# Kernel tuning notes

Hardware: AMD Instinct MI355X
Metric: run time of the kernel (lower is better)

## Reference

```python
import jax, jax.numpy as jnp
import numpy as np

C = 64
N_H = 4
N_WIN = 16
WIN_L = 8   # compressor window length (overlapped)
WIN_S = 4   # compressor stride -> T//4 blocks


def _rms(x, eps=1e-6):
    return x * jax.lax.rsqrt(jnp.mean(x * x, axis=-1, keepdims=True) + eps)


def _rope(x, negate=False):
    # x: (..., L, D); rotate-half RoPE over positions 0..L-1
    L, D = x.shape[-2], x.shape[-1]
    half = D // 2
    inv_freq = 1.0 / (10000.0 ** (jnp.arange(half, dtype=x.dtype) / half))
    ang = jnp.arange(L, dtype=x.dtype)[:, None] * inv_freq  # (L, half)
    if negate:
        ang = -ang
    cos, sin = jnp.cos(ang), jnp.sin(ang)
    x1, x2 = x[..., :half], x[..., half:]
    return jnp.concatenate([x1 * cos - x2 * sin, x1 * sin + x2 * cos], axis=-1)


def _compress(H, W):
    # overlapped token compressor: windows of WIN_L, stride WIN_S, zero-pad tail
    B, T, d = H.shape
    Tc = T // WIN_S
    Hp = jnp.pad(H, ((0, 0), (0, WIN_L - WIN_S), (0, 0)))
    idx = WIN_S * jnp.arange(Tc)[:, None] + jnp.arange(WIN_L)[None, :]  # (Tc, WIN_L)
    win = Hp[:, idx]                       # (B, Tc, WIN_L, d)
    return win.reshape(B, Tc, WIN_L * d) @ W  # (B, Tc, out)


def setup_inputs() -> dict:
    key = jax.random.key(0)
    ks = jax.random.split(key, 11)
    B, T, d = 2, 2048, 256

    def w(k, shape, fan):
        return jax.random.normal(k, shape, jnp.float32) / np.float32(np.sqrt(fan))

    H = jax.random.normal(ks[0], (B, T, d), jnp.float32)
    return {
        'H': H,
        'Wc_comp': w(ks[1], (WIN_L * d, C), WIN_L * d),
        'Wc_idx': w(ks[2], (WIN_L * d, 32), WIN_L * d),
        'W_DQ': w(ks[3], (d, 64), d),
        'W_IUQ': w(ks[4], (64, 4 * 32), 64),
        'W_w': w(ks[5], (64, 4), 64),
        'W_Q': w(ks[6], (d, N_H * C), d),
        'W_KV': w(ks[7], (d, C), d),
        'g_q': jnp.ones((N_H, C), jnp.float32),
        'g_k': jnp.ones((C,), jnp.float32),
        'g_v': jnp.ones((C,), jnp.float32),
        'Wg0': w(ks[8], (2 * C, 64), 2 * C),
        'bg0': jnp.zeros((64,), jnp.float32),
        'Wg1': w(ks[9], (2 * C, 64), 2 * C),
        'bg1': jnp.zeros((64,), jnp.float32),
        'Wout': w(ks[10], (128, d), 128),
        'bout': jnp.zeros((d,), jnp.float32),
    }


def reference(H, Wc_comp, Wc_idx, W_DQ, W_IUQ, W_w, W_Q, W_KV,
              g_q, g_k, g_v, Wg0, bg0, Wg1, bg1, Wout, bout):
    B, T, d = H.shape
    Tc = T // 4
    k_top = min(8, Tc)

    # ---- lightning indexer ----
    H_dc = H @ W_DQ                                   # (B,T,64)
    Q_I = (H_dc @ W_IUQ).reshape(B, T, 4, 32)         # (B,T,4,32)
    W_Iw = (H_dc @ W_w)[..., None]                    # (B,T,4,1)
    K_I = _compress(H, Wc_idx)                        # (B,Tc,32)
    dot = jnp.einsum('bthc,bsc->bths', Q_I, K_I)      # (B,T,4,Tc)
    I_ts = (W_Iw * jax.nn.relu(dot)).sum(axis=2)      # (B,T,Tc)

    t = jnp.arange(T)[:, None]
    s = jnp.arange(Tc)[None, :]
    mask_I = jnp.where(4 * s <= t, 0.0, -jnp.inf)     # (T,Tc) causal over blocks
    _, topk_idx = jax.lax.top_k(I_ts + mask_I, k_top)  # (B,T,k)
    bI = jnp.arange(B)[:, None, None]
    tI = jnp.arange(T)[None, :, None]
    M_comp = jnp.full((B, T, Tc), -jnp.inf).at[bI, tI, topk_idx].set(0.0)

    # ---- compressed + sliding KV ----
    KV = jnp.concatenate([_compress(H, Wc_comp), H @ W_KV], axis=1)  # (B,Tc+T,C)

    Q = (H @ W_Q).reshape(B, T, N_H, C).transpose(0, 2, 1, 3)        # (B,nh,T,C)
    Q = _rms(Q) * g_q[None, :, None, :]
    K = _rms(KV) * g_k
    V = _rms(KV) * g_v
    Q = _rope(Q)
    K = _rope(K)
    V = _rope(V)

    S = jnp.einsum('bhtc,bsc->bhts', Q, K) / np.float32(np.sqrt(C))  # (B,nh,T,Tc+T)

    S_comp = S[..., :Tc] + M_comp[:, None]
    rel = t - jnp.arange(T)[None, :]
    mask_slide = jnp.where((rel >= 0) & (rel < N_WIN), 0.0, -jnp.inf)  # (T,T)
    S_slide = S[..., Tc:] + mask_slide

    P = jax.nn.softmax(jnp.concatenate([S_comp, S_slide], axis=-1), axis=-1)
    O = jnp.einsum('bhts,bsc->bhtc', P, V)            # (B,nh,T,C)
    O = _rope(O, negate=True)

    O0 = O[:, :2].transpose(0, 2, 1, 3).reshape(B, T, 2 * C)
    O1 = O[:, 2:].transpose(0, 2, 1, 3).reshape(B, T, 2 * C)
    p_all = jnp.concatenate([O0 @ Wg0 + bg0, O1 @ Wg1 + bg1], axis=-1)
    return p_all @ Wout + bout
```

## Files before the change

kernel.cpp:

```cpp
#include <hip/hip_runtime.h>
#include <hip/hip_bf16.h>
#include <math.h>

#define T_DIM 2048
#define B_DIM 2
#define D_DIM 256
#define TC 512
#define KV_LEN 2560

typedef __attribute__((ext_vector_type(8))) short bf16x8;
typedef __attribute__((ext_vector_type(4))) float f32x4;
typedef unsigned short ush;

__device__ __forceinline__ float wave_sum64(float v) {
#pragma unroll
    for (int off = 32; off > 0; off >>= 1) v += __shfl_xor(v, off, 64);
    return v;
}

__device__ __forceinline__ float rope_angle(int pos, int j) {
    float inv = powf(10000.0f, -(float)j * (1.0f / 32.0f));
    return (float)pos * inv;
}

__global__ __launch_bounds__(256) void k_prep(
    const float* __restrict__ H, const float* __restrict__ W_Q,
    const float* __restrict__ W_KV, const float* __restrict__ W_DQ,
    const float* __restrict__ W_IUQ, const float* __restrict__ W_w,
    const float* __restrict__ Wc_comp, const float* __restrict__ Wc_idx,
    const float* __restrict__ Wg0, const float* __restrict__ bg0,
    const float* __restrict__ Wg1, const float* __restrict__ bg1,
    const float* __restrict__ Wout, const float* __restrict__ bout,
    ush* __restrict__ Ap, ush* __restrict__ Bp, ush* __restrict__ Bc,
    ush* __restrict__ Bo, float* __restrict__ biascomb)
{
    int gid = blockIdx.x * 256 + threadIdx.x;
    float vals[8];
    ush* dst;
    bool lo_part;

    if (gid < 262144) {
        int tile = gid >> 10;
        int c = (gid >> 6) & 15;
        int l = gid & 63;
        int bt = tile * 16 + (l & 15);
        int kb = (c & 7) * 32 + (l >> 4) * 8;
        const float* src = H + (size_t)bt * 256 + kb;
#pragma unroll
        for (int j = 0; j < 8; ++j) vals[j] = src[j];
        lo_part = (c >= 8);
        dst = Ap + (size_t)gid * 8;
    } else if (gid < 294912) {
        int g = gid - 262144;
        int tile = g >> 10;
        int c = (g >> 6) & 15;
        int l = g & 63;
        int n = tile * 16 + (l & 15);
        int kb = (c & 7) * 32 + (l >> 4) * 8;
#pragma unroll
        for (int j = 0; j < 8; ++j) {
            int k = kb + j;
            float w;
            if (n < 256)      w = W_Q[(size_t)k * 256 + n];
            else if (n < 320) w = W_KV[(size_t)k * 64 + (n - 256)];
            else if (n < 448) {
                w = 0.f;
                for (int i = 0; i < 64; ++i)
                    w = fmaf(W_DQ[(size_t)k * 64 + i], W_IUQ[(size_t)i * 128 + (n - 320)], w);
            } else if (n < 452) {
                w = 0.f;
                for (int i = 0; i < 64; ++i)
                    w = fmaf(W_DQ[(size_t)k * 64 + i], W_w[(size_t)i * 4 + (n - 448)], w);
            } else {
                w = 0.f;
            }
            vals[j] = w;
        }
        lo_part = (c >= 8);
        dst = Bp + (size_t)g * 8;
    } else if (gid < 344064) {
        int g = gid - 294912;
        int tile = g >> 13;
        int c = (g >> 6) & 127;
        int l = g & 63;
        int n = tile * 16 + (l & 15);
        int k2b = (c & 63) * 32 + (l >> 4) * 8;
#pragma unroll
        for (int j = 0; j < 8; ++j) {
            int k = k2b + j;
            vals[j] = (n < 64) ? Wc_comp[(size_t)k * 64 + n]
                               : Wc_idx[(size_t)k * 32 + (n - 64)];
        }
        lo_part = (c >= 64);
        dst = Bc + (size_t)g * 8;
    } else if (gid < 409600) {
        int g = gid - 344064;
        int k = g >> 8;
        int n = g & 255;
        float acc = 0.f;
        if (k < 128) {
            for (int i = 0; i < 64; ++i)
                acc = fmaf(Wg0[k * 64 + i], Wout[(size_t)i * 256 + n], acc);
        } else {
            for (int i = 0; i < 64; ++i)
                acc = fmaf(Wg1[(k - 128) * 64 + i], Wout[(size_t)(64 + i) * 256 + n], acc);
        }
        __hip_bfloat16 hb = __float2bfloat16(acc);
        float hif = __bfloat162float(hb);
        __hip_bfloat16 lb = __float2bfloat16(acc - hif);
        int tile = n >> 4;
        int chi = k >> 5;
        int lane2 = (n & 15) + 16 * ((k >> 3) & 3);
        int j = k & 7;
        Bo[(size_t)(tile * 16 + chi) * 512 + lane2 * 8 + j] = *(ush*)&hb;
        Bo[(size_t)(tile * 16 + chi + 8) * 512 + lane2 * 8 + j] = *(ush*)&lb;
        return;
    } else if (gid < 409856) {
        int n = gid - 409600;
        float acc = bout[n];
        for (int i = 0; i < 64; ++i) {
            acc = fmaf(bg0[i], Wout[(size_t)i * 256 + n], acc);
            acc = fmaf(bg1[i], Wout[(size_t)(64 + i) * 256 + n], acc);
        }
        biascomb[n] = acc;
        return;
    } else {
        return;
    }

    bf16x8 out8;
#pragma unroll
    for (int j = 0; j < 8; ++j) {
        float x = vals[j];
        __hip_bfloat16 hb = __float2bfloat16(x);
        if (!lo_part) {
            out8[j] = *(short*)&hb;
        } else {
            float hif = __bfloat162float(hb);
            __hip_bfloat16 lb = __float2bfloat16(x - hif);
            out8[j] = *(short*)&lb;
        }
    }
    *(bf16x8*)dst = out8;
}

__global__ __launch_bounds__(64) void k_mfma(
    const ush* __restrict__ Ap, const ush* __restrict__ Bp,
    const ush* __restrict__ Bc,
    const float* __restrict__ g_q, const float* __restrict__ g_k,
    const float* __restrict__ g_v,
    float* __restrict__ Pre, float* __restrict__ Prec_part,
    float* __restrict__ Qr, float* __restrict__ Kbuf, float* __restrict__ Vbuf)
{
    int lane = threadIdx.x;
    int mrow = lane & 15;
    int q = lane >> 4;

    if (blockIdx.x < 512) {
        int p = blockIdx.x;
        int m0 = (p >> 2) * 32;
        int nq = p & 3;
        int n0 = nq * 128;
        int at0 = (m0 >> 4) * 16;
        int bt0n = (n0 >> 4) * 16;

        f32x4 acc[2][8];
#pragma unroll
        for (int mt = 0; mt < 2; ++mt)
#pragma unroll
            for (int nt = 0; nt < 8; ++nt) acc[mt][nt] = (f32x4){0.f, 0.f, 0.f, 0.f};

        for (int c = 0; c < 8; ++c) {
            bf16x8 ahi[2], alo[2], bhi[8], blo[8];
#pragma unroll
            for (int mt = 0; mt < 2; ++mt) {
                ahi[mt] = *(const bf16x8*)(Ap + (size_t)((at0 + mt * 16) + c) * 512 + lane * 8);
                alo[mt] = *(const bf16x8*)(Ap + (size_t)((at0 + mt * 16) + 8 + c) * 512 + lane * 8);
            }
#pragma unroll
            for (int nt = 0; nt < 8; ++nt) {
                bhi[nt] = *(const bf16x8*)(Bp + (size_t)((bt0n + nt * 16) + c) * 512 + lane * 8);
                blo[nt] = *(const bf16x8*)(Bp + (size_t)((bt0n + nt * 16) + 8 + c) * 512 + lane * 8);
            }
#pragma unroll
            for (int mt = 0; mt < 2; ++mt)
#pragma unroll
                for (int nt = 0; nt < 8; ++nt) {
                    acc[mt][nt] = __builtin_amdgcn_mfma_f32_16x16x32_bf16(ahi[mt], bhi[nt], acc[mt][nt], 0, 0, 0);
                    acc[mt][nt] = __builtin_amdgcn_mfma_f32_16x16x32_bf16(ahi[mt], blo[nt], acc[mt][nt], 0, 0, 0);
                    acc[mt][nt] = __builtin_amdgcn_mfma_f32_16x16x32_bf16(alo[mt], bhi[nt], acc[mt][nt], 0, 0, 0);
                }
        }

        if (nq < 2) {
            int h0 = nq * 2, h1 = nq * 2 + 1;
#pragma unroll
            for (int mt = 0; mt < 2; ++mt)
#pragma unroll
                for (int reg = 0; reg < 4; ++reg) {
                    int bt = m0 + 16 * mt + 4 * q + reg;
                    int t = bt & 2047;
                    float ss0 = 0.f, ss1 = 0.f;
#pragma unroll
                    for (int k = 0; k < 4; ++k) {
                        float v0 = acc[mt][k][reg];
                        float v1 = acc[mt][4 + k][reg];
                        ss0 = fmaf(v0, v0, ss0);
                        ss1 = fmaf(v1, v1, ss1);
                    }
#pragma unroll
                    for (int off = 1; off <= 8; off <<= 1) {
                        ss0 += __shfl_xor(ss0, off, 64);
                        ss1 += __shfl_xor(ss1, off, 64);
                    }
                    float sc0 = rsqrtf(ss0 * (1.0f / 64.0f) + 1e-6f);
                    float sc1 = rsqrtf(ss1 * (1.0f / 64.0f) + 1e-6f);
#pragma unroll
                    for (int k = 0; k < 2; ++k) {
                        int jj = 16 * k + mrow;
                        float sa, ca;
                        sincosf(rope_angle(t, jj), &sa, &ca);
                        {
                            float x1 = acc[mt][k][reg] * sc0 * g_q[h0 * 64 + jj];
                            float x2 = acc[mt][k + 2][reg] * sc0 * g_q[h0 * 64 + 32 + jj];
                            Qr[(size_t)bt * 256 + h0 * 64 + jj] = fmaf(x1, ca, -x2 * sa);
                            Qr[(size_t)bt * 256 + h0 * 64 + 32 + jj] = fmaf(x1, sa, x2 * ca);
                        }
                        {
                            float x1 = acc[mt][4 + k][reg] * sc1 * g_q[h1 * 64 + jj];
                            float x2 = acc[mt][4 + k + 2][reg] * sc1 * g_q[h1 * 64 + 32 + jj];
                            Qr[(size_t)bt * 256 + h1 * 64 + jj] = fmaf(x1, ca, -x2 * sa);
                            Qr[(size_t)bt * 256 + h1 * 64 + 32 + jj] = fmaf(x1, sa, x2 * ca);
                        }
                    }
                }
        } else if (nq == 2) {
#pragma unroll
            for (int mt = 0; mt < 2; ++mt)
#pragma unroll
                for (int reg = 0; reg < 4; ++reg) {
                    int bt = m0 + 16 * mt + 4 * q + reg;
                    int b = bt >> 11;
                    int t = bt & 2047;
                    float ss = 0.f;
#pragma unroll
                    for (int k = 0; k < 4; ++k) {
                        float v = acc[mt][k][reg];
                        ss = fmaf(v, v, ss);
                    }
#pragma unroll
                    for (int off = 1; off <= 8; off <<= 1) ss += __shfl_xor(ss, off, 64);
                    float sc = rsqrtf(ss * (1.0f / 64.0f) + 1e-6f);
                    int pos = TC + t;
                    size_t base = ((size_t)b * KV_LEN + pos) * 64;
#pragma unroll
                    for (int k = 0; k < 2; ++k) {
                        int jj = 16 * k + mrow;
                        float sa, ca;
                        sincosf(rope_angle(pos, jj), &sa, &ca);
                        float k1 = acc[mt][k][reg] * sc * g_k[jj];
                        float k2 = acc[mt][k + 2][reg] * sc * g_k[32 + jj];
                        float v1 = acc[mt][k][reg] * sc * g_v[jj];
                        float v2 = acc[mt][k + 2][reg] * sc * g_v[32 + jj];
                        Kbuf[base + jj] = fmaf(k1, ca, -k2 * sa);
                        Kbuf[base + 32 + jj] = fmaf(k1, sa, k2 * ca);
                        Vbuf[base + jj] = fmaf(v1, ca, -v2 * sa);
                        Vbuf[base + 32 + jj] = fmaf(v1, sa, v2 * ca);
                    }
#pragma unroll
                    for (int nt = 4; nt < 8; ++nt)
                        Pre[(size_t)bt * 512 + n0 + 16 * nt + mrow] = acc[mt][nt][reg];
                }
        } else {
#pragma unroll
            for (int mt = 0; mt < 2; ++mt)
#pragma unroll
                for (int nt = 0; nt < 8; ++nt)
#pragma unroll
                    for (int reg = 0; reg < 4; ++reg)
                        Pre[(size_t)(m0 + 16 * mt + 4 * q + reg) * 512 + n0 + 16 * nt + mrow] =
                            acc[mt][nt][reg];
        }
    } else {
        int cb = blockIdx.x - 512;
        int m0 = (cb >> 2) * 32;
        int q4 = cb & 3;
        int bb = m0 >> 9;

        f32x4 acc[2][6];
#pragma unroll
        for (int mt = 0; mt < 2; ++mt)
#pragma unroll
            for (int nt = 0; nt < 6; ++nt) acc[mt][nt] = (f32x4){0.f, 0.f, 0.f, 0.f};

        for (int cl = 0; cl < 16; ++cl) {
            int cc = q4 * 16 + cl;
            int k2b = cc * 32 + q * 8;
            int row_off = k2b >> 8;
            int kcb = k2b & 255;
            int chA = kcb >> 5;
            int lsub = (kcb >> 3) & 3;

            bf16x8 ahi[2], alo[2], bhi[6], blo[6];
#pragma unroll
            for (int mt = 0; mt < 2; ++mt) {
                int s_loc = (m0 & 511) + 16 * mt + mrow;
                int r_loc = 4 * s_loc + row_off;
                int r_glob = bb * 2048 + r_loc;
                int tileA = r_glob >> 4;
                int laneA = (r_glob & 15) + 16 * lsub;
                bf16x8 h8 = *(const bf16x8*)(Ap + (size_t)(tileA * 16 + chA) * 512 + laneA * 8);
                bf16x8 l8 = *(const bf16x8*)(Ap + (size_t)(tileA * 16 + chA + 8) * 512 + laneA * 8);
                if (r_loc >= T_DIM) {
#pragma unroll
                    for (int j = 0; j < 8; ++j) { h8[j] = 0; l8[j] = 0; }
                }
                ahi[mt] = h8;
                alo[mt] = l8;
            }
#pragma unroll
            for (int nt = 0; nt < 6; ++nt) {
                bhi[nt] = *(const bf16x8*)(Bc + (size_t)(nt * 128 + cc) * 512 + lane * 8);
                blo[nt] = *(const bf16x8*)(Bc + (size_t)(nt * 128 + 64 + cc) * 512 + lane * 8);
            }
#pragma unroll
            for (int mt = 0; mt < 2; ++mt)
#pragma unroll
                for (int nt = 0; nt < 6; ++nt) {
                    acc[mt][nt] = __builtin_amdgcn_mfma_f32_16x16x32_bf16(ahi[mt], bhi[nt], acc[mt][nt], 0, 0, 0);
                    acc[mt][nt] = __builtin_amdgcn_mfma_f32_16x16x32_bf16(ahi[mt], blo[nt], acc[mt][nt], 0, 0, 0);
                    acc[mt][nt] = __builtin_amdgcn_mfma_f32_16x16x32_bf16(alo[mt], bhi[nt], acc[mt][nt], 0, 0, 0);
                }
        }

        float* dst = Prec_part + (size_t)q4 * (1024 * 96);
#pragma unroll
        for (int mt = 0; mt < 2; ++mt)
#pragma unroll
            for (int nt = 0; nt < 6; ++nt)
#pragma unroll
                for (int reg = 0; reg < 4; ++reg)
                    dst[(size_t)(m0 + 16 * mt + 4 * q + reg) * 96 + 16 * nt + mrow] =
                        acc[mt][nt][reg];
    }
}

__global__ __launch_bounds__(256) void k_epi(
    const float* __restrict__ Prec_part,
    const float* __restrict__ g_k, const float* __restrict__ g_v,
    float* __restrict__ KIbuf, float* __restrict__ Kbuf, float* __restrict__ Vbuf)
{
    int tid = threadIdx.x;
    int wv = tid >> 6;
    int lane = tid & 63;
    int sg = blockIdx.x * 4 + wv;
    int b = sg >> 9;
    int s = sg & 511;

    const float* p0 = Prec_part + (size_t)sg * 96;
    float kvv = p0[lane] + p0[98304 + lane] + p0[2 * 98304 + lane] + p0[3 * 98304 + lane];

    float ss = wave_sum64(kvv * kvv);
    float sc = rsqrtf(ss * (1.0f / 64.0f) + 1e-6f);
    float kk = kvv * sc * g_k[lane];
    float vv = kvv * sc * g_v[lane];
    int j = lane & 31;
    float sa, ca;
    sincosf(rope_angle(s, j), &sa, &ca);
    float pk = __shfl_xor(kk, 32, 64);
    float pv = __shfl_xor(vv, 32, 64);
    float ko = (lane < 32) ? fmaf(kk, ca, -pk * sa) : fmaf(pk, sa, kk * ca);
    float vo = (lane < 32) ? fmaf(vv, ca, -pv * sa) : fmaf(pv, sa, vv * ca);
    size_t off = ((size_t)b * KV_LEN + s) * 64 + lane;
    Kbuf[off] = ko;
    Vbuf[off] = vo;

    if (lane < 32) {
        float a = p0[64 + lane] + p0[98304 + 64 + lane] +
                  p0[2 * 98304 + 64 + lane] + p0[3 * 98304 + 64 + lane];
        KIbuf[((size_t)b * TC + s) * 32 + lane] = a;
    }
}

__global__ __launch_bounds__(256) void k_score_topk(
    const float* __restrict__ Pre, const float* __restrict__ KIbuf,
    int* __restrict__ topk)
{
    int tid = threadIdx.x;
    int wv = tid >> 6;
    int lane = tid & 63;
    int bt0 = blockIdx.x * 4;
    int bt = bt0 + wv;
    int b = bt >> 11;
    int t = bt & 2047;

    __shared__ float sQ[4][128];
    __shared__ float sw[4][4];
    __shared__ float sKI[64 * 33];

    const float* pr = Pre + (size_t)bt * 512;
    sQ[wv][lane] = pr[320 + lane];
    sQ[wv][64 + lane] = pr[384 + lane];
    if (lane < 4) sw[wv][lane] = pr[448 + lane];

    const float* KIb = KIbuf + (size_t)b * TC * 32;
    int smax = t >> 2;
    int smax_blk = ((bt0 + 3) & 2047) >> 2;

    float vals[8];
#pragma unroll
    for (int r = 0; r < 8; ++r) vals[r] = -INFINITY;

    for (int r = 0; r < 8; ++r) {
        if (r * 64 > smax_blk) break;
        __syncthreads();
        for (int i = tid; i < 512; i += 256) {
            int row = i >> 3;
            int cseg = (i & 7) * 4;
            float4 v = *(const float4*)(KIb + (size_t)(r * 64 + row) * 32 + cseg);
            float* dstp = &sKI[row * 33 + cseg];
            dstp[0] = v.x; dstp[1] = v.y; dstp[2] = v.z; dstp[3] = v.w;
        }
        __syncthreads();

        int s = r * 64 + lane;
        if (s <= smax) {
            float dd0 = 0.f, dd1 = 0.f, dd2 = 0.f, dd3 = 0.f;
#pragma unroll
            for (int c = 0; c < 32; ++c) {
                float kv = sKI[lane * 33 + c];
                dd0 = fmaf(sQ[wv][c], kv, dd0);
                dd1 = fmaf(sQ[wv][32 + c], kv, dd1);
                dd2 = fmaf(sQ[wv][64 + c], kv, dd2);
                dd3 = fmaf(sQ[wv][96 + c], kv, dd3);
            }
            vals[r] = sw[wv][0] * fmaxf(dd0, 0.f) + sw[wv][1] * fmaxf(dd1, 0.f) +
                      sw[wv][2] * fmaxf(dd2, 0.f) + sw[wv][3] * fmaxf(dd3, 0.f);
        }
    }

    unsigned consumed = 0u;
    for (int k2 = 0; k2 < 8; ++k2) {
        float bv = -INFINITY;
        int bi = 0x7fffffff;
#pragma unroll
        for (int r = 0; r < 8; ++r) {
            if (!(consumed & (1u << r))) {
                int s = lane + 64 * r;
                float v = vals[r];
                if (v > bv || (v == bv && s < bi)) { bv = v; bi = s; }
            }
        }
#pragma unroll
        for (int off = 1; off < 64; off <<= 1) {
            float ov = __shfl_xor(bv, off, 64);
            int oi = __shfl_xor(bi, off, 64);
            if (ov > bv || (ov == bv && oi < bi)) { bv = ov; bi = oi; }
        }
        if ((bi & 63) == lane) consumed |= 1u << (bi >> 6);
        if (lane == 0) topk[(size_t)bt * 8 + k2] = bi;
    }
}

__global__ __launch_bounds__(1024) void k_attn(
    const float* __restrict__ Qr, const float* __restrict__ Kbuf,
    const float* __restrict__ Vbuf, const int* __restrict__ topk,
    float* __restrict__ Obuf)
{
    int tid = threadIdx.x;
    int lt = tid >> 8;
    int t256 = tid & 255;
    int h = t256 >> 6;
    int lane = tid & 63;
    int bt0 = blockIdx.x * 4;
    int bt = bt0 + lt;
    int b = bt >> 11;
    int t = bt & 2047;
    int t0 = bt0 & 2047;

    __shared__ float sKV[102 * 65];
    __shared__ float sQ[4][256];
    __shared__ int sPos[4][8];
    __shared__ float sP[4][4][24];

    sQ[lt][t256] = Qr[(size_t)bt * 256 + t256];
    if (t256 < 8) sPos[lt][t256] = topk[(size_t)bt * 8 + t256];
    __syncthreads();

    for (int i = tid; i < 1632; i += 1024) {
        int row = i >> 4;
        int seg = (i & 15) << 2;
        const float* srcbase;
        bool ok = true;
        if (row < 38) {
            int idx = (row < 19) ? row : row - 19;
            int sp = t0 - 15 + idx;
            ok = (sp >= 0);
            srcbase = ((row < 19) ? Kbuf : Vbuf) +
                      ((size_t)b * KV_LEN + TC + sp) * 64;
        } else {
            int r = row - 38;
            int ltt = r >> 4;
            int slot = r & 15;
            int pos = sPos[ltt][slot & 7];
            srcbase = ((slot < 8) ? Kbuf : Vbuf) +
                      ((size_t)b * KV_LEN + pos) * 64;
        }
        if (ok) {
            float4 v = *(const float4*)(srcbase + seg);
            float* d = &sKV[row * 65 + seg];
            d[0] = v.x; d[1] = v.y; d[2] = v.z; d[3] = v.w;
        }
    }
    __syncthreads();

    float scv = -INFINITY;
    if (lane < 24) {
        int krow;
        bool valid;
        if (lane < 8) { krow = 38 + lt * 16 + lane; valid = true; }
        else          { krow = lt + 23 - lane; valid = (t - (lane - 8) >= 0); }
        if (valid) {
            float dd = 0.f;
#pragma unroll
            for (int c = 0; c < 64; ++c)
                dd = fmaf(sQ[lt][h * 64 + c], sKV[krow * 65 + c], dd);
            scv = dd * 0.125f;
        }
    }
    float m = scv;
#pragma unroll
    for (int off = 1; off < 64; off <<= 1) m = fmaxf(m, __shfl_xor(m, off, 64));
    float p = expf(scv - m);
    if (scv == -INFINITY) p = 0.f;
    float l = p;
#pragma unroll
    for (int off = 1; off < 64; off <<= 1) l += __shfl_xor(l, off, 64);
    p /= l;
    if (lane < 24) sP[lt][h][lane] = p;

    float o = 0.f;
#pragma unroll
    for (int j2 = 0; j2 < 8; ++j2) {
        int vrow = 38 + lt * 16 + 8 + j2;
        o = fmaf(sP[lt][h][j2], sKV[vrow * 65 + lane], o);
    }
#pragma unroll
    for (int j2 = 8; j2 < 24; ++j2) {
        if (t - (j2 - 8) >= 0) {
            int vrow = 19 + (lt + 23 - j2);
            o = fmaf(sP[lt][h][j2], sKV[vrow * 65 + lane], o);
        }
    }

    int j = lane & 31;
    float sa, ca;
    sincosf(rope_angle(t, j), &sa, &ca);
    float prt = __shfl_xor(o, 32, 64);
    float oo = (lane < 32) ? fmaf(o, ca, prt * sa) : fmaf(-prt, sa, o * ca);
    Obuf[(size_t)bt * 256 + h * 64 + lane] = oo;
}

__global__ __launch_bounds__(64) void k_out(
    const float* __restrict__ Obuf, const ush* __restrict__ Bo,
    const float* __restrict__ biascomb, float* __restrict__ out)
{
    int lane = threadIdx.x;
    int mrow = lane & 15;
    int q = lane >> 4;
    int p = blockIdx.x;
    int m0 = (p >> 2) * 32;
    int n0 = (p & 3) * 64;
    int bt0n = (n0 >> 4) * 16;

    f32x4 acc[2][4];
#pragma unroll
    for (int mt = 0; mt < 2; ++mt)
#pragma unroll
        for (int nt = 0; nt < 4; ++nt) acc[mt][nt] = (f32x4){0.f, 0.f, 0.f, 0.f};

    for (int c = 0; c < 8; ++c) {
        bf16x8 ahi[2], alo[2], bhi[4], blo[4];
#pragma unroll
        for (int mt = 0; mt < 2; ++mt) {
            const float* src = Obuf + (size_t)(m0 + 16 * mt + mrow) * 256 + c * 32 + 8 * q;
            float4 x0 = *(const float4*)src;
            float4 x1 = *(const float4*)(src + 4);
            float xs[8] = {x0.x, x0.y, x0.z, x0.w, x1.x, x1.y, x1.z, x1.w};
#pragma unroll
            for (int j = 0; j < 8; ++j) {
                __hip_bfloat16 hb = __float2bfloat16(xs[j]);
                float hif = __bfloat162float(hb);
                __hip_bfloat16 lb = __float2bfloat16(xs[j] - hif);
                ahi[mt][j] = *(short*)&hb;
                alo[mt][j] = *(short*)&lb;
            }
        }
#pragma unroll
        for (int nt = 0; nt < 4; ++nt) {
            bhi[nt] = *(const bf16x8*)(Bo + (size_t)((bt0n + nt * 16) + c) * 512 + lane * 8);
            blo[nt] = *(const bf16x8*)(Bo + (size_t)((bt0n + nt * 16) + 8 + c) * 512 + lane * 8);
        }
#pragma unroll
        for (int mt = 0; mt < 2; ++mt)
#pragma unroll
            for (int nt = 0; nt < 4; ++nt) {
                acc[mt][nt] = __builtin_amdgcn_mfma_f32_16x16x32_bf16(ahi[mt], bhi[nt], acc[mt][nt], 0, 0, 0);
                acc[mt][nt] = __builtin_amdgcn_mfma_f32_16x16x32_bf16(ahi[mt], blo[nt], acc[mt][nt], 0, 0, 0);
                acc[mt][nt] = __builtin_amdgcn_mfma_f32_16x16x32_bf16(alo[mt], bhi[nt], acc[mt][nt], 0, 0, 0);
            }
    }

#pragma unroll
    for (int mt = 0; mt < 2; ++mt)
#pragma unroll
        for (int nt = 0; nt < 4; ++nt) {
            float bia = biascomb[n0 + 16 * nt + mrow];
#pragma unroll
            for (int reg = 0; reg < 4; ++reg)
                out[(size_t)(m0 + 16 * mt + 4 * q + reg) * 256 + n0 + 16 * nt + mrow] =
                    acc[mt][nt][reg] + bia;
        }
}

extern "C" void kernel_launch(void* const* d_in, const int* in_sizes, int n_in,
                              void* d_out, int out_size, void* d_ws, size_t ws_size,
                              hipStream_t stream) {
    const float* H       = (const float*)d_in[0];
    const float* Wc_comp = (const float*)d_in[1];
    const float* Wc_idx  = (const float*)d_in[2];
    const float* W_DQ    = (const float*)d_in[3];
    const float* W_IUQ   = (const float*)d_in[4];
    const float* W_w     = (const float*)d_in[5];
    const float* W_Q     = (const float*)d_in[6];
    const float* W_KV    = (const float*)d_in[7];
    const float* g_q     = (const float*)d_in[8];
    const float* g_k     = (const float*)d_in[9];
    const float* g_v     = (const float*)d_in[10];
    const float* Wg0     = (const float*)d_in[11];
    const float* bg0     = (const float*)d_in[12];
    const float* Wg1     = (const float*)d_in[13];
    const float* bg1     = (const float*)d_in[14];
    const float* Wout    = (const float*)d_in[15];
    const float* bout    = (const float*)d_in[16];

    float* ws = (float*)d_ws;
    float* Qr   = ws;
    float* KI   = ws + 1048576;
    float* Kb   = ws + 1081344;
    float* Vb   = ws + 1409024;
    float* Pre  = ws + 1736704;
    float* Prec = ws + 3833856;
    float* Obuf = ws + 4227072;
    int* topkb  = (int*)(ws + 5275648);
    ush* Ap = (ush*)(ws + 5308416);
    ush* Bp = (ush*)(ws + 8454144);
    ush* Bc = (ush*)(ws + 8585216);
    ush* Bo = (ush*)(ws + 8781824);
    float* biascomb = ws + 8847360;

    float* outp = (float*)d_out;

    hipLaunchKernelGGL(k_prep, dim3(1601), dim3(256), 0, stream,
                       H, W_Q, W_KV, W_DQ, W_IUQ, W_w, Wc_comp, Wc_idx,
                       Wg0, bg0, Wg1, bg1, Wout, bout,
                       Ap, Bp, Bc, Bo, biascomb);
    hipLaunchKernelGGL(k_mfma, dim3(640), dim3(64), 0, stream,
                       Ap, Bp, Bc, g_q, g_k, g_v, Pre, Prec, Qr, Kb, Vb);
    hipLaunchKernelGGL(k_epi, dim3(256), dim3(256), 0, stream,
                       Prec, g_k, g_v, KI, Kb, Vb);
    hipLaunchKernelGGL(k_score_topk, dim3(1024), dim3(256), 0, stream,
                       Pre, KI, topkb);
    hipLaunchKernelGGL(k_attn, dim3(1024), dim3(1024), 0, stream,
                       Qr, Kb, Vb, topkb, Obuf);
    hipLaunchKernelGGL(k_out, dim3(512), dim3(64), 0, stream,
                       Obuf, Bo, biascomb, outp);
}
```

Measured before the change: 176.8 us.

## Fuse compressor epilogue into MFMA kernel and drop split-K partials

```diff
diff --git a/kernel.cpp b/kernel.cpp
--- a/kernel.cpp
+++ b/kernel.cpp
@@ -11,12 +11,6 @@
 typedef __attribute__((ext_vector_type(8))) short bf16x8;
 typedef __attribute__((ext_vector_type(4))) float f32x4;
 typedef unsigned short ush;
-
-__device__ __forceinline__ float wave_sum64(float v) {
-#pragma unroll
-    for (int off = 32; off > 0; off >>= 1) v += __shfl_xor(v, off, 64);
-    return v;
-}
 
 __device__ __forceinline__ float rope_angle(int pos, int j) {
     float inv = powf(10000.0f, -(float)j * (1.0f / 32.0f));
@@ -149,7 +143,7 @@
     const ush* __restrict__ Bc,
     const float* __restrict__ g_q, const float* __restrict__ g_k,
     const float* __restrict__ g_v,
-    float* __restrict__ Pre, float* __restrict__ Prec_part,
+    float* __restrict__ Pre, float* __restrict__ KIbuf,
     float* __restrict__ Qr, float* __restrict__ Kbuf, float* __restrict__ Vbuf)
 {
     int lane = threadIdx.x;
@@ -283,8 +277,7 @@
         }
     } else {
         int cb = blockIdx.x - 512;
-        int m0 = (cb >> 2) * 32;
-        int q4 = cb & 3;
+        int m0 = cb * 32;
         int bb = m0 >> 9;
 
         f32x4 acc[2][6];
@@ -293,8 +286,7 @@
 #pragma unroll
             for (int nt = 0; nt < 6; ++nt) acc[mt][nt] = (f32x4){0.f, 0.f, 0.f, 0.f};
 
-        for (int cl = 0; cl < 16; ++cl) {
-            int cc = q4 * 16 + cl;
+        for (int cc = 0; cc < 64; ++cc) {
             int k2b = cc * 32 + q * 8;
             int row_off = k2b >> 8;
             int kcb = k2b & 255;
@@ -333,52 +325,40 @@
                 }
         }
 
-        float* dst = Prec_part + (size_t)q4 * (1024 * 96);
 #pragma unroll
         for (int mt = 0; mt < 2; ++mt)
 #pragma unroll
-            for (int nt = 0; nt < 6; ++nt)
-#pragma unroll
-                for (int reg = 0; reg < 4; ++reg)
-                    dst[(size_t)(m0 + 16 * mt + 4 * q + reg) * 96 + 16 * nt + mrow] =
-                        acc[mt][nt][reg];
-    }
-}
-
-__global__ __launch_bounds__(256) void k_epi(
-    const float* __restrict__ Prec_part,
-    const float* __restrict__ g_k, const float* __restrict__ g_v,
-    float* __restrict__ KIbuf, float* __restrict__ Kbuf, float* __restrict__ Vbuf)
-{
-    int tid = threadIdx.x;
-    int wv = tid >> 6;
-    int lane = tid & 63;
-    int sg = blockIdx.x * 4 + wv;
-    int b = sg >> 9;
-    int s = sg & 511;
-
-    const float* p0 = Prec_part + (size_t)sg * 96;
-    float kvv = p0[lane] + p0[98304 + lane] + p0[2 * 98304 + lane] + p0[3 * 98304 + lane];
-
-    float ss = wave_sum64(kvv * kvv);
-    float sc = rsqrtf(ss * (1.0f / 64.0f) + 1e-6f);
-    float kk = kvv * sc * g_k[lane];
-    float vv = kvv * sc * g_v[lane];
-    int j = lane & 31;
-    float sa, ca;
-    sincosf(rope_angle(s, j), &sa, &ca);
-    float pk = __shfl_xor(kk, 32, 64);
-    float pv = __shfl_xor(vv, 32, 64);
-    float ko = (lane < 32) ? fmaf(kk, ca, -pk * sa) : fmaf(pk, sa, kk * ca);
-    float vo = (lane < 32) ? fmaf(vv, ca, -pv * sa) : fmaf(pv, sa, vv * ca);
-    size_t off = ((size_t)b * KV_LEN + s) * 64 + lane;
-    Kbuf[off] = ko;
-    Vbuf[off] = vo;
-
-    if (lane < 32) {
-        float a = p0[64 + lane] + p0[98304 + 64 + lane] +
-                  p0[2 * 98304 + 64 + lane] + p0[3 * 98304 + 64 + lane];
-        KIbuf[((size_t)b * TC + s) * 32 + lane] = a;
+            for (int reg = 0; reg < 4; ++reg) {
+                int sg = m0 + 16 * mt + 4 * q + reg;
+                int b = sg >> 9;
+                int s = sg & 511;
+                float ss = 0.f;
+#pragma unroll
+                for (int k = 0; k < 4; ++k) {
+                    float v = acc[mt][k][reg];
+                    ss = fmaf(v, v, ss);
+                }
+#pragma unroll
+                for (int off = 1; off <= 8; off <<= 1) ss += __shfl_xor(ss, off, 64);
+                float sc = rsqrtf(ss * (1.0f / 64.0f) + 1e-6f);
+                size_t base = ((size_t)b * KV_LEN + s) * 64;
+#pragma unroll
+                for (int k = 0; k < 2; ++k) {
+                    int jj = 16 * k + mrow;
+                    float sa, ca;
+                    sincosf(rope_angle(s, jj), &sa, &ca);
+                    float k1 = acc[mt][k][reg] * sc * g_k[jj];
+                    float k2 = acc[mt][k + 2][reg] * sc * g_k[32 + jj];
+                    float v1 = acc[mt][k][reg] * sc * g_v[jj];
+                    float v2 = acc[mt][k + 2][reg] * sc * g_v[32 + jj];
+                    Kbuf[base + jj] = fmaf(k1, ca, -k2 * sa);
+                    Kbuf[base + 32 + jj] = fmaf(k1, sa, k2 * ca);
+                    Vbuf[base + jj] = fmaf(v1, ca, -v2 * sa);
+                    Vbuf[base + 32 + jj] = fmaf(v1, sa, v2 * ca);
+                }
+                KIbuf[((size_t)b * TC + s) * 32 + mrow] = acc[mt][4][reg];
+                KIbuf[((size_t)b * TC + s) * 32 + 16 + mrow] = acc[mt][5][reg];
+            }
     }
 }
 
@@ -650,7 +630,6 @@
     float* Kb   = ws + 1081344;
     float* Vb   = ws + 1409024;
     float* Pre  = ws + 1736704;
-    float* Prec = ws + 3833856;
     float* Obuf = ws + 4227072;
     int* topkb  = (int*)(ws + 5275648);
     ush* Ap = (ush*)(ws + 5308416);
@@ -665,10 +644,8 @@
                        H, W_Q, W_KV, W_DQ, W_IUQ, W_w, Wc_comp, Wc_idx,
                        Wg0, bg0, Wg1, bg1, Wout, bout,
                        Ap, Bp, Bc, Bo, biascomb);
-    hipLaunchKernelGGL(k_mfma, dim3(640), dim3(64), 0, stream,
-                       Ap, Bp, Bc, g_q, g_k, g_v, Pre, Prec, Qr, Kb, Vb);
-    hipLaunchKernelGGL(k_epi, dim3(256), dim3(256), 0, stream,
-                       Prec, g_k, g_v, KI, Kb, Vb);
+    hipLaunchKernelGGL(k_mfma, dim3(544), dim3(64), 0, stream,
+                       Ap, Bp, Bc, g_q, g_k, g_v, Pre, KI, Qr, Kb, Vb);
     hipLaunchKernelGGL(k_score_topk, dim3(1024), dim3(256), 0, stream,
                        Pre, KI, topkb);
     hipLaunchKernelGGL(k_attn, dim3(1024), dim3(1024), 0, stream,
```

Result: slower. 209.8 us (+18.6%).
